# Optimization experiments

Measured on AMD Instinct MI355X. Metric: run time of the kernel, lower is better.

The kernel has to match this reference:

```python
import jax, jax.numpy as jnp
import numpy as np

N_NODES = 50000
N_EDGES = 800000
IN_FEATS = 128
OUT_FEATS = 128
N_REL = 3


def setup_inputs() -> dict:
    key = jax.random.key(0)
    k1, k2, k3, k4, k5, k6 = jax.random.split(key, 6)
    feature = jax.random.normal(k1, (N_NODES, IN_FEATS), dtype=jnp.float32)
    # kaiming_uniform-ish scale for faithfulness of magnitude
    bound = float(np.sqrt(6.0 / IN_FEATS))
    weight = jax.random.uniform(k2, (N_REL, IN_FEATS, OUT_FEATS), dtype=jnp.float32,
                                minval=-bound, maxval=bound)
    norm = jax.random.uniform(k3, (N_EDGES,), dtype=jnp.float32)
    src = jax.random.randint(k4, (N_EDGES,), 0, N_NODES)
    dst = jax.random.randint(k5, (N_EDGES,), 0, N_NODES)
    rel_type = jax.random.randint(k6, (N_EDGES,), 0, N_REL)
    return {"feature": feature, "weight": weight, "norm": norm,
            "src": src, "dst": dst, "rel_type": rel_type}


def reference(feature, weight, norm, src, dst, rel_type):
    # Per-edge message: norm_e * (x[src_e] @ W[rel_type_e]).
    # Since there are only 3 relations, transform ALL nodes once per relation
    # (grouped GEMM: [3, N, in] x [3, in, out]) then gather the right
    # (relation, src) row per edge -- same math, avoids per-edge bmm.
    hr = jnp.einsum('ni,rio->rno', feature, weight)       # [3, N, out]
    msg = hr[rel_type, src] * norm[:, None]               # [E, out]
    # fn.sum reduce -> scatter-sum into destination nodes (zero if no in-edges)
    h = jax.ops.segment_sum(msg, dst, num_segments=feature.shape[0])  # [N, out]
    return jax.nn.relu(h)
```

## Files before the change

### kernel.cpp

```cpp
#include <hip/hip_runtime.h>
#include <stdint.h>

#define NFEAT  128
#define NREL   3
#define BINCAP 5120

typedef short short8 __attribute__((ext_vector_type(8)));
typedef float f32x4  __attribute__((ext_vector_type(4)));
typedef unsigned int u32x4 __attribute__((ext_vector_type(4)));

__device__ __forceinline__ uint32_t f2bf(float x) {
    uint32_t u = __builtin_bit_cast(uint32_t, x);
    uint32_t r = (u + 0x7FFFu + ((u >> 16) & 1u)) >> 16;
    return r & 0xFFFFu;
}
__device__ __forceinline__ float bf_lo(uint32_t v) {
    return __builtin_bit_cast(float, v << 16);
}
__device__ __forceinline__ float bf_hi(uint32_t v) {
    return __builtin_bit_cast(float, v & 0xFFFF0000u);
}

__global__ __launch_bounds__(256) void k_prep(
    const float* __restrict__ W, uint16_t* __restrict__ Wt,
    int* __restrict__ bincursor, int WBn)
{
    const int t = threadIdx.x;
    if (blockIdx.x == (unsigned)WBn) {
        bincursor[t] = 0;
        return;
    }
    const int tid = blockIdx.x * 256 + t;
    if (tid >= NREL * NFEAT * 16) return;
    const int k8 = tid & 15;
    const int o  = (tid >> 4) & 127;
    const int r  = tid >> 11;
    const float* Wr = W + (size_t)r * NFEAT * NFEAT;
    uint32_t pk[4];
    #pragma unroll
    for (int q = 0; q < 4; q++) {
        float lo = Wr[(size_t)(k8 * 8 + q * 2)     * NFEAT + o];
        float hi = Wr[(size_t)(k8 * 8 + q * 2 + 1) * NFEAT + o];
        pk[q] = f2bf(lo) | (f2bf(hi) << 16);
    }
    uint4 v = make_uint4(pk[0], pk[1], pk[2], pk[3]);
    *reinterpret_cast<uint4*>(&Wt[(size_t)r * NFEAT * NFEAT + (size_t)o * NFEAT + k8 * 8]) = v;
}

__global__ __launch_bounds__(256) void k_gemm_mfma(
    const float* __restrict__ feat, const uint16_t* __restrict__ Wt,
    uint16_t* __restrict__ hr, int N)
{
    __shared__ uint16_t ldsA[64 * 128];
    __shared__ uint16_t ldsB[128 * 128];

    const int t    = threadIdx.x;
    const int lane = t & 63;
    const int w    = t >> 6;
    const int n0   = blockIdx.x * 64;

    {
        const int kq = t & 15;
        const int rq = t >> 4;
        #pragma unroll
        for (int rr = 0; rr < 4; rr++) {
            const int row = rr * 16 + rq;
            const int n = n0 + row;
            uint4 pk = make_uint4(0, 0, 0, 0);
            if (n < N) {
                const float4* p = reinterpret_cast<const float4*>(&feat[(size_t)n * NFEAT + kq * 8]);
                float4 v0 = p[0], v1 = p[1];
                pk.x = f2bf(v0.x) | (f2bf(v0.y) << 16);
                pk.y = f2bf(v0.z) | (f2bf(v0.w) << 16);
                pk.z = f2bf(v1.x) | (f2bf(v1.y) << 16);
                pk.w = f2bf(v1.z) | (f2bf(v1.w) << 16);
            }
            uint32_t byte = (uint32_t)(row * 256 + kq * 16) ^ ((uint32_t)(row & 7) << 4);
            *reinterpret_cast<uint4*>(reinterpret_cast<char*>(ldsA) + byte) = pk;
        }
    }

    const int rowf = lane & 15;
    const int kb   = lane >> 4;

    for (int r = 0; r < NREL; r++) {
        {
            const int kq = t & 15;
            const int rq = t >> 4;
            const uint16_t* Wr = Wt + (size_t)r * NFEAT * NFEAT;
            #pragma unroll
            for (int rr = 0; rr < 8; rr++) {
                const int row = rr * 16 + rq;
                uint4 v = *reinterpret_cast<const uint4*>(&Wr[(size_t)row * NFEAT + kq * 8]);
                uint32_t byte = (uint32_t)(row * 256 + kq * 16) ^ ((uint32_t)(row & 7) << 4);
                *reinterpret_cast<uint4*>(reinterpret_cast<char*>(ldsB) + byte) = v;
            }
        }
        __syncthreads();

        short8 a[4];
        {
            const int row = w * 16 + rowf;
            #pragma unroll
            for (int ks = 0; ks < 4; ks++) {
                uint32_t byte = (uint32_t)(row * 256 + ks * 64 + kb * 16) ^ ((uint32_t)(row & 7) << 4);
                a[ks] = *reinterpret_cast<const short8*>(reinterpret_cast<char*>(ldsA) + byte);
            }
        }

        f32x4 acc[8];
        #pragma unroll
        for (int cf = 0; cf < 8; cf++) acc[cf] = (f32x4){0.f, 0.f, 0.f, 0.f};

        #pragma unroll
        for (int cf = 0; cf < 8; cf++) {
            const int col = cf * 16 + rowf;
            #pragma unroll
            for (int ks = 0; ks < 4; ks++) {
                uint32_t byte = (uint32_t)(col * 256 + ks * 64 + kb * 16) ^ ((uint32_t)(col & 7) << 4);
                short8 b = *reinterpret_cast<const short8*>(reinterpret_cast<char*>(ldsB) + byte);
                acc[cf] = __builtin_amdgcn_mfma_f32_16x16x32_bf16(a[ks], b, acc[cf], 0, 0, 0);
            }
        }

        #pragma unroll
        for (int cf = 0; cf < 8; cf++) {
            #pragma unroll
            for (int j = 0; j < 4; j++) {
                const int n = n0 + w * 16 + kb * 4 + j;
                if (n < N)
                    hr[((size_t)r * N + n) * NFEAT + cf * 16 + rowf] = (uint16_t)f2bf(acc[cf][j]);
            }
        }
        __syncthreads();
    }
}

__global__ __launch_bounds__(256) void k_binfill(
    const int* __restrict__ dst, const int* __restrict__ src,
    const int* __restrict__ rel, const float* __restrict__ norm,
    int* __restrict__ bincursor, uint2* __restrict__ binbuf, int N, int E)
{
    __shared__ int hist[256];
    __shared__ int base[256];
    __shared__ int rank[256];
    const int t = threadIdx.x;
    const int e0 = blockIdx.x * 2048;

    hist[t] = 0;
    __syncthreads();

    int myBin[8], myDl[8];
    #pragma unroll
    for (int j = 0; j < 8; j++) {
        int e = e0 + t + j * 256;
        int b = -1, dl = 0;
        if (e < E) {
            int d = dst[e];
            b = d >> 8;
            dl = d & 255;
            atomicAdd(&hist[b], 1);
        }
        myBin[j] = b;
        myDl[j] = dl;
    }
    __syncthreads();

    int h = hist[t];
    if (h > 0) base[t] = atomicAdd(&bincursor[t], h);
    rank[t] = 0;
    __syncthreads();

    #pragma unroll
    for (int j = 0; j < 8; j++) {
        int e = e0 + t + j * 256;
        if (myBin[j] >= 0) {
            int slot = base[myBin[j]] + atomicAdd(&rank[myBin[j]], 1);
            if (slot < BINCAP) {
                uint32_t rowidx = (uint32_t)(rel[e] * N + src[e]);
                uint32_t px = rowidx | ((uint32_t)myDl[j] << 18);
                binbuf[(size_t)myBin[j] * BINCAP + slot] =
                    make_uint2(px, __builtin_bit_cast(uint32_t, norm[e]));
            }
        }
    }
}

__global__ __launch_bounds__(256) void k_binsort(
    const uint2* __restrict__ binbuf, const int* __restrict__ bincursor,
    uint2* __restrict__ meta, uint2* __restrict__ offs, int N)
{
    __shared__ int sm[256];
    __shared__ int cur[256];
    const int b = blockIdx.x;
    const int t = threadIdx.x;
    const int base = b * BINCAP;
    int cnt = bincursor[b];
    if (cnt > BINCAP) cnt = BINCAP;

    sm[t] = 0;
    __syncthreads();
    for (int i = t; i < cnt; i += 256) {
        uint2 r = binbuf[base + i];
        atomicAdd(&sm[(r.x >> 18) & 255], 1);
    }
    __syncthreads();
    int v = sm[t];
    __syncthreads();
    sm[t] = v;
    __syncthreads();
    for (int s = 1; s < 256; s <<= 1) {
        int a = (t >= s) ? sm[t - s] : 0;
        __syncthreads();
        sm[t] += a;
        __syncthreads();
    }
    int excl = sm[t] - v;
    int n = b * 256 + t;
    if (n < N) offs[n] = make_uint2(base + excl, base + excl + v);
    cur[t] = excl;
    __syncthreads();

    for (int i = t; i < cnt; i += 256) {
        uint2 r = binbuf[base + i];
        int dl = (r.x >> 18) & 255;
        int p = atomicAdd(&cur[dl], 1);
        meta[base + p] = make_uint2(r.x & 0x3FFFFu, r.y);
    }
}

__global__ __launch_bounds__(256) void k_aggregate(
    const uint16_t* __restrict__ hr, const uint2* __restrict__ offs,
    const uint64_t* __restrict__ meta, float* __restrict__ out, int N)
{
    const int wid  = threadIdx.x >> 6;
    const int lane = threadIdx.x & 63;
    const int n = blockIdx.x * 4 + wid;
    if (n >= N) return;

    const uint2 se = offs[n];
    int idx = (int)se.x;
    const int end = (int)se.y;

    const int g = lane >> 4;
    const int q = lane & 15;
    const char* hrb = reinterpret_cast<const char*>(hr) + q * 16;

    float a0 = 0.f, a1 = 0.f, a2 = 0.f, a3 = 0.f;
    float a4 = 0.f, a5 = 0.f, a6 = 0.f, a7 = 0.f;

    for (; idx + 7 < end; idx += 8) {
        uint64_t m0 = __builtin_nontemporal_load(&meta[idx + g]);
        uint64_t m1 = __builtin_nontemporal_load(&meta[idx + 4 + g]);
        u32x4 v0 = *reinterpret_cast<const u32x4*>(hrb + ((size_t)(uint32_t)m0 << 8));
        u32x4 v1 = *reinterpret_cast<const u32x4*>(hrb + ((size_t)(uint32_t)m1 << 8));
        float w0 = __builtin_bit_cast(float, (uint32_t)(m0 >> 32));
        float w1 = __builtin_bit_cast(float, (uint32_t)(m1 >> 32));
        a0 += w0 * bf_lo(v0.x); a1 += w0 * bf_hi(v0.x);
        a2 += w0 * bf_lo(v0.y); a3 += w0 * bf_hi(v0.y);
        a4 += w0 * bf_lo(v0.z); a5 += w0 * bf_hi(v0.z);
        a6 += w0 * bf_lo(v0.w); a7 += w0 * bf_hi(v0.w);
        a0 += w1 * bf_lo(v1.x); a1 += w1 * bf_hi(v1.x);
        a2 += w1 * bf_lo(v1.y); a3 += w1 * bf_hi(v1.y);
        a4 += w1 * bf_lo(v1.z); a5 += w1 * bf_hi(v1.z);
        a6 += w1 * bf_lo(v1.w); a7 += w1 * bf_hi(v1.w);
    }
    for (; idx + 3 < end; idx += 4) {
        uint64_t m0 = __builtin_nontemporal_load(&meta[idx + g]);
        u32x4 v0 = *reinterpret_cast<const u32x4*>(hrb + ((size_t)(uint32_t)m0 << 8));
        float w0 = __builtin_bit_cast(float, (uint32_t)(m0 >> 32));
        a0 += w0 * bf_lo(v0.x); a1 += w0 * bf_hi(v0.x);
        a2 += w0 * bf_lo(v0.y); a3 += w0 * bf_hi(v0.y);
        a4 += w0 * bf_lo(v0.z); a5 += w0 * bf_hi(v0.z);
        a6 += w0 * bf_lo(v0.w); a7 += w0 * bf_hi(v0.w);
    }
    if (idx + g < end) {
        uint64_t m0 = __builtin_nontemporal_load(&meta[idx + g]);
        u32x4 v0 = *reinterpret_cast<const u32x4*>(hrb + ((size_t)(uint32_t)m0 << 8));
        float w0 = __builtin_bit_cast(float, (uint32_t)(m0 >> 32));
        a0 += w0 * bf_lo(v0.x); a1 += w0 * bf_hi(v0.x);
        a2 += w0 * bf_lo(v0.y); a3 += w0 * bf_hi(v0.y);
        a4 += w0 * bf_lo(v0.z); a5 += w0 * bf_hi(v0.z);
        a6 += w0 * bf_lo(v0.w); a7 += w0 * bf_hi(v0.w);
    }

    a0 += __shfl_xor(a0, 16); a1 += __shfl_xor(a1, 16);
    a2 += __shfl_xor(a2, 16); a3 += __shfl_xor(a3, 16);
    a4 += __shfl_xor(a4, 16); a5 += __shfl_xor(a5, 16);
    a6 += __shfl_xor(a6, 16); a7 += __shfl_xor(a7, 16);
    a0 += __shfl_xor(a0, 32); a1 += __shfl_xor(a1, 32);
    a2 += __shfl_xor(a2, 32); a3 += __shfl_xor(a3, 32);
    a4 += __shfl_xor(a4, 32); a5 += __shfl_xor(a5, 32);
    a6 += __shfl_xor(a6, 32); a7 += __shfl_xor(a7, 32);

    if (g == 0) {
        f32x4 o0, o1;
        o0[0] = fmaxf(a0, 0.f); o0[1] = fmaxf(a1, 0.f);
        o0[2] = fmaxf(a2, 0.f); o0[3] = fmaxf(a3, 0.f);
        o1[0] = fmaxf(a4, 0.f); o1[1] = fmaxf(a5, 0.f);
        o1[2] = fmaxf(a6, 0.f); o1[3] = fmaxf(a7, 0.f);
        f32x4* po = reinterpret_cast<f32x4*>(&out[(size_t)n * NFEAT + q * 8]);
        __builtin_nontemporal_store(o0, po);
        __builtin_nontemporal_store(o1, po + 1);
    }
}

extern "C" void kernel_launch(void* const* d_in, const int* in_sizes, int n_in,
                              void* d_out, int out_size, void* d_ws, size_t ws_size,
                              hipStream_t stream)
{
    const float* feat = (const float*)d_in[0];
    const float* W    = (const float*)d_in[1];
    const float* norm = (const float*)d_in[2];
    const int*   src  = (const int*)d_in[3];
    const int*   dst  = (const int*)d_in[4];
    const int*   rel  = (const int*)d_in[5];
    float* out = (float*)d_out;

    const int N = in_sizes[0] / NFEAT;
    const int E = in_sizes[2];
    const int NBINS = (N + 255) / 256;
    const int HB  = (E + 2047) / 2048;
    const int WBn = (NREL * NFEAT * 16 + 255) / 256;

    char* ws = (char*)d_ws;
    size_t off = 0;
    auto alloc = [&](size_t bytes) -> char* {
        char* p = ws + off;
        off += (bytes + 63) & ~(size_t)63;
        return p;
    };
    uint16_t* hr    = (uint16_t*)alloc((size_t)NREL * N * NFEAT * 2);
    uint16_t* Wt    = (uint16_t*)alloc((size_t)NREL * NFEAT * NFEAT * 2);
    int* bincursor  = (int*)alloc(256 * 4);
    uint2* offs     = (uint2*)alloc((size_t)N * 8);
    uint2* meta     = (uint2*)alloc((size_t)NBINS * BINCAP * 8);
    (void)ws_size;

    uint2* binbuf = (uint2*)d_out;

    k_prep<<<WBn + 1, 256, 0, stream>>>(W, Wt, bincursor, WBn);
    k_binfill<<<HB, 256, 0, stream>>>(dst, src, rel, norm, bincursor, binbuf, N, E);
    k_binsort<<<NBINS, 256, 0, stream>>>(binbuf, bincursor, meta, offs, N);
    k_gemm_mfma<<<(N + 63) / 64, 256, 0, stream>>>(feat, Wt, hr, N);
    k_aggregate<<<(N + 3) / 4, 256, 0, stream>>>(hr, offs, (const uint64_t*)meta, out, N);
}
```

Baseline: 96.37 us.

## Double GEMM row tile and stage binfill writes through LDS for coalescing

The GEMM now handles 128 rows per block, with each wave computing two 16-row fragments. Each B fragment read from LDS therefore feeds two MFMAs, halving B-operand LDS traffic and the number of W reloads per row. Separately, binfill now counting-sorts each block's 2048 edges by bin in shared memory using a prefix scan. It then writes contiguous runs to the global bin buffer instead of scattered 8-byte stores. This adds LDS use (more occupancy pressure in both kernels) and a scan with many barriers.

```diff
diff --git a/kernel.cpp b/kernel.cpp
--- a/kernel.cpp
+++ b/kernel.cpp
@@ -51,19 +51,19 @@
     const float* __restrict__ feat, const uint16_t* __restrict__ Wt,
     uint16_t* __restrict__ hr, int N)
 {
-    __shared__ uint16_t ldsA[64 * 128];
+    __shared__ uint16_t ldsA[128 * 128];
     __shared__ uint16_t ldsB[128 * 128];
 
     const int t    = threadIdx.x;
     const int lane = t & 63;
     const int w    = t >> 6;
-    const int n0   = blockIdx.x * 64;
+    const int n0   = blockIdx.x * 128;
 
     {
         const int kq = t & 15;
         const int rq = t >> 4;
         #pragma unroll
-        for (int rr = 0; rr < 4; rr++) {
+        for (int rr = 0; rr < 8; rr++) {
             const int row = rr * 16 + rq;
             const int n = n0 + row;
             uint4 pk = make_uint4(0, 0, 0, 0);
@@ -98,19 +98,22 @@
         }
         __syncthreads();
 
-        short8 a[4];
-        {
-            const int row = w * 16 + rowf;
+        short8 a[2][4];
+        #pragma unroll
+        for (int rf = 0; rf < 2; rf++) {
+            const int row = w * 32 + rf * 16 + rowf;
             #pragma unroll
             for (int ks = 0; ks < 4; ks++) {
                 uint32_t byte = (uint32_t)(row * 256 + ks * 64 + kb * 16) ^ ((uint32_t)(row & 7) << 4);
-                a[ks] = *reinterpret_cast<const short8*>(reinterpret_cast<char*>(ldsA) + byte);
-            }
-        }
-
-        f32x4 acc[8];
-        #pragma unroll
-        for (int cf = 0; cf < 8; cf++) acc[cf] = (f32x4){0.f, 0.f, 0.f, 0.f};
+                a[rf][ks] = *reinterpret_cast<const short8*>(reinterpret_cast<char*>(ldsA) + byte);
+            }
+        }
+
+        f32x4 acc[2][8];
+        #pragma unroll
+        for (int rf = 0; rf < 2; rf++)
+            #pragma unroll
+            for (int cf = 0; cf < 8; cf++) acc[rf][cf] = (f32x4){0.f, 0.f, 0.f, 0.f};
 
         #pragma unroll
         for (int cf = 0; cf < 8; cf++) {
@@ -119,17 +122,21 @@
             for (int ks = 0; ks < 4; ks++) {
                 uint32_t byte = (uint32_t)(col * 256 + ks * 64 + kb * 16) ^ ((uint32_t)(col & 7) << 4);
                 short8 b = *reinterpret_cast<const short8*>(reinterpret_cast<char*>(ldsB) + byte);
-                acc[cf] = __builtin_amdgcn_mfma_f32_16x16x32_bf16(a[ks], b, acc[cf], 0, 0, 0);
-            }
-        }
-
-        #pragma unroll
-        for (int cf = 0; cf < 8; cf++) {
-            #pragma unroll
-            for (int j = 0; j < 4; j++) {
-                const int n = n0 + w * 16 + kb * 4 + j;
-                if (n < N)
-                    hr[((size_t)r * N + n) * NFEAT + cf * 16 + rowf] = (uint16_t)f2bf(acc[cf][j]);
+                acc[0][cf] = __builtin_amdgcn_mfma_f32_16x16x32_bf16(a[0][ks], b, acc[0][cf], 0, 0, 0);
+                acc[1][cf] = __builtin_amdgcn_mfma_f32_16x16x32_bf16(a[1][ks], b, acc[1][cf], 0, 0, 0);
+            }
+        }
+
+        #pragma unroll
+        for (int rf = 0; rf < 2; rf++) {
+            #pragma unroll
+            for (int cf = 0; cf < 8; cf++) {
+                #pragma unroll
+                for (int j = 0; j < 4; j++) {
+                    const int n = n0 + w * 32 + rf * 16 + kb * 4 + j;
+                    if (n < N)
+                        hr[((size_t)r * N + n) * NFEAT + cf * 16 + rowf] = (uint16_t)f2bf(acc[rf][cf][j]);
+                }
             }
         }
         __syncthreads();
@@ -142,47 +149,64 @@
     int* __restrict__ bincursor, uint2* __restrict__ binbuf, int N, int E)
 {
     __shared__ int hist[256];
-    __shared__ int base[256];
-    __shared__ int rank[256];
+    __shared__ int sm[256];
+    __shared__ int binstart[256];
+    __shared__ int gbase[256];
+    __shared__ uint2 buf[2048];
+    __shared__ uint8_t binof[2048];
     const int t = threadIdx.x;
     const int e0 = blockIdx.x * 2048;
 
     hist[t] = 0;
     __syncthreads();
 
-    int myBin[8], myDl[8];
+    int myBin[8], myLoc[8];
+    uint2 myRec[8];
     #pragma unroll
     for (int j = 0; j < 8; j++) {
-        int e = e0 + t + j * 256;
-        int b = -1, dl = 0;
+        int e = e0 + j * 256 + t;
+        myBin[j] = -1;
         if (e < E) {
             int d = dst[e];
-            b = d >> 8;
-            dl = d & 255;
-            atomicAdd(&hist[b], 1);
-        }
-        myBin[j] = b;
-        myDl[j] = dl;
-    }
-    __syncthreads();
-
-    int h = hist[t];
-    if (h > 0) base[t] = atomicAdd(&bincursor[t], h);
-    rank[t] = 0;
+            int b = d >> 8;
+            myBin[j] = b;
+            myLoc[j] = atomicAdd(&hist[b], 1);
+            uint32_t rowidx = (uint32_t)(rel[e] * N + src[e]);
+            myRec[j] = make_uint2(rowidx | ((uint32_t)(d & 255) << 18),
+                                  __builtin_bit_cast(uint32_t, norm[e]));
+        }
+    }
+    __syncthreads();
+
+    const int v = hist[t];
+    sm[t] = v;
+    __syncthreads();
+    for (int s = 1; s < 256; s <<= 1) {
+        int a = (t >= s) ? sm[t - s] : 0;
+        __syncthreads();
+        sm[t] += a;
+        __syncthreads();
+    }
+    binstart[t] = sm[t] - v;
+    gbase[t] = (v > 0) ? atomicAdd(&bincursor[t], v) : 0;
     __syncthreads();
 
     #pragma unroll
     for (int j = 0; j < 8; j++) {
-        int e = e0 + t + j * 256;
         if (myBin[j] >= 0) {
-            int slot = base[myBin[j]] + atomicAdd(&rank[myBin[j]], 1);
-            if (slot < BINCAP) {
-                uint32_t rowidx = (uint32_t)(rel[e] * N + src[e]);
-                uint32_t px = rowidx | ((uint32_t)myDl[j] << 18);
-                binbuf[(size_t)myBin[j] * BINCAP + slot] =
-                    make_uint2(px, __builtin_bit_cast(uint32_t, norm[e]));
-            }
-        }
+            int pos = binstart[myBin[j]] + myLoc[j];
+            buf[pos] = myRec[j];
+            binof[pos] = (uint8_t)myBin[j];
+        }
+    }
+    __syncthreads();
+
+    const int total = binstart[255] + hist[255];
+    for (int i = t; i < total; i += 256) {
+        int b = binof[i];
+        int slot = gbase[b] + (i - binstart[b]);
+        if (slot < BINCAP)
+            binbuf[(size_t)b * BINCAP + slot] = buf[i];
     }
 }
 
@@ -342,6 +366,6 @@
     k_prep<<<WBn + 1, 256, 0, stream>>>(W, Wt, bincursor, WBn);
     k_binfill<<<HB, 256, 0, stream>>>(dst, src, rel, norm, bincursor, binbuf, N, E);
     k_binsort<<<NBINS, 256, 0, stream>>>(binbuf, bincursor, meta, offs, N);
-    k_gemm_mfma<<<(N + 63) / 64, 256, 0, stream>>>(feat, Wt, hr, N);
+    k_gemm_mfma<<<(N + 127) / 128, 256, 0, stream>>>(feat, Wt, hr, N);
     k_aggregate<<<(N + 3) / 4, 256, 0, stream>>>(hr, offs, (const uint64_t*)meta, out, N);
 }
```

Result: faster. 92.52 us (-4.0%).
